# Performance work log

Measured on AMD Instinct MI355X. Metric: run time of the kernel, lower is better.

## Reference

```python
import jax, jax.numpy as jnp
import numpy as np

E, H, B, S = 1024, 16, 8, 512
D = E // H
GRU_BIAS = 2.0  # config['gru_bias']
LN_EPS = 1e-5


def _pos_encoding(seq_len, dim):
    # Transformer-XL style relative positions seq_len-1 .. 0
    pos = jnp.arange(seq_len - 1, -1, -1, dtype=jnp.float32)
    inv_freq = 1.0 / (10000.0 ** (jnp.arange(0, dim, 2, dtype=jnp.float32) / dim))
    ang = pos[:, None] * inv_freq[None, :]              # [S, E/2]
    return jnp.concatenate([jnp.sin(ang), jnp.cos(ang)], axis=-1)  # [S, E]


def _layer_norm(x, g, b):
    m = x.mean(-1, keepdims=True)
    v = ((x - m) ** 2).mean(-1, keepdims=True)
    return (x - m) * jax.lax.rsqrt(v + LN_EPS) * g + b


def _rel_shift(x):
    # x: [B, H, S, S] -> Transformer-XL relative shift
    b, h, s, _ = x.shape
    x = jnp.pad(x, ((0, 0), (0, 0), (0, 0), (1, 0)))
    x = x.reshape(b, h, s + 1, s)[:, :, 1:, :]
    return x


def _gru_gate(x, y, Wr, Ur, Wz, Uz, Wg, Ug):
    # GTrXL gating: r, z gates + candidate h; z biased toward identity by GRU_BIAS
    r = jax.nn.sigmoid(y @ Wr.T + x @ Ur.T)
    z = jax.nn.sigmoid(y @ Wz.T + x @ Uz.T - GRU_BIAS)
    h = jnp.tanh(y @ Wg.T + (r * x) @ Ug.T)
    return (1.0 - z) * x + z * h


def setup_inputs() -> dict:
    rng = jax.random.key(0)
    ks = iter(jax.random.split(rng, 64))
    W = lambda *shape: jax.random.normal(next(ks), shape, jnp.float32) * 0.02
    inp = {
        "query": jax.random.normal(next(ks), (B, S, E), jnp.float32),
        "key": jax.random.normal(next(ks), (B, S, E), jnp.float32),
        "value": jax.random.normal(next(ks), (B, S, E), jnp.float32),
        "mask": jnp.tril(jnp.ones((S, S), dtype=bool)),
        "ln1_g": jnp.ones((E,), jnp.float32), "ln1_b": jnp.zeros((E,), jnp.float32),
        "ln2_g": jnp.ones((E,), jnp.float32), "ln2_b": jnp.zeros((E,), jnp.float32),
        "Wq": W(E, E), "bq": jnp.zeros((E,), jnp.float32),
        "Wk": W(E, E), "bk": jnp.zeros((E,), jnp.float32),
        "Wv": W(E, E), "bv": jnp.zeros((E,), jnp.float32),
        "Wp": W(E, E),
        "Wo": W(E, E), "bo": jnp.zeros((E,), jnp.float32),
        "u_bias": W(H, D), "v_bias": W(H, D),
        "g1_Wr": W(E, E), "g1_Ur": W(E, E), "g1_Wz": W(E, E),
        "g1_Uz": W(E, E), "g1_Wg": W(E, E), "g1_Ug": W(E, E),
        "g2_Wr": W(E, E), "g2_Ur": W(E, E), "g2_Wz": W(E, E),
        "g2_Uz": W(E, E), "g2_Wg": W(E, E), "g2_Ug": W(E, E),
        "fc_W": W(E, E), "fc_b": jnp.zeros((E,), jnp.float32),
    }
    return inp


def reference(query, key, value, mask,
              ln1_g, ln1_b, ln2_g, ln2_b,
              Wq, bq, Wk, bk, Wv, bv, Wp, Wo, bo, u_bias, v_bias,
              g1_Wr, g1_Ur, g1_Wz, g1_Uz, g1_Wg, g1_Ug,
              g2_Wr, g2_Ur, g2_Wz, g2_Uz, g2_Wg, g2_Ug,
              fc_W, fc_b):
    b, s, e = query.shape
    norm_q = _layer_norm(query, ln1_g, ln1_b)
    norm_k = _layer_norm(key, ln1_g, ln1_b)

    q = (norm_q @ Wq.T + bq).reshape(b, s, H, D)
    k = (norm_k @ Wk.T + bk).reshape(b, s, H, D)
    v = (norm_k @ Wv.T + bv).reshape(b, s, H, D)
    r = (_pos_encoding(s, e) @ Wp.T).reshape(s, H, D)      # relative pos keys

    # content term (q + u) k^T and position term (q + v) R^T with rel-shift
    AC = jnp.einsum('bshd,bthd->bhst', q + u_bias, k)
    BD = _rel_shift(jnp.einsum('bshd,thd->bhst', q + v_bias, r))
    score = (AC + BD) / jnp.sqrt(jnp.float32(D))
    score = jnp.where(mask[None, None, :, :], score, jnp.float32(-1e9))
    attn = jax.nn.softmax(score, axis=-1)
    Y = jnp.einsum('bhst,bthd->bshd', attn, v).reshape(b, s, e) @ Wo.T + bo

    out = _gru_gate(query, Y, g1_Wr, g1_Ur, g1_Wz, g1_Uz, g1_Wg, g1_Ug)
    Ef = jax.nn.relu(_layer_norm(out, ln2_g, ln2_b) @ fc_W.T + fc_b)
    out = _gru_gate(out, Ef, g2_Wr, g2_Ur, g2_Wz, g2_Uz, g2_Wg, g2_Ug)
    return out
```

## Files before the change

### kernel.cpp

```cpp
#include <hip/hip_runtime.h>

typedef unsigned short u16;
typedef __attribute__((ext_vector_type(8))) short short8;
typedef __attribute__((ext_vector_type(4))) float f32x4;

#define DEVFN __device__ __forceinline__

constexpr int Bc = 8, Sc = 512, Ec = 1024, Hc = 16, Dc = 64;

DEVFN u16 f2b(float f) {
  union { float f; unsigned u; } a; a.f = f;
  unsigned u = a.u;
  u += 0x7fffu + ((u >> 16) & 1u);
  return (u16)(u >> 16);
}
DEVFN float b2f(u16 h) {
  union { unsigned u; float f; } a; a.u = ((unsigned)h) << 16; return a.f;
}
DEVFN unsigned pack2(float a, float b) {
  return (unsigned)f2b(a) | ((unsigned)f2b(b) << 16);
}
DEVFN float wred_sum(float v) {
  #pragma unroll
  for (int o = 32; o; o >>= 1) v += __shfl_xor(v, o, 64);
  return v;
}
DEVFN void gload16(const void* g, void* l) {
  __builtin_amdgcn_global_load_lds(
      (const __attribute__((address_space(1))) void*)g,
      (__attribute__((address_space(3))) void*)l, 16, 0, 0);
}

struct PtrBundle { const float* src[18]; u16* dst[18]; };

__global__ __launch_bounds__(256) void cvtw_kernel(PtrBundle pb)
{
  int w = blockIdx.y;
  int i = blockIdx.x * 256 + threadIdx.x;
  float4 v = ((const float4*)pb.src[w])[i];
  uint2 o; o.x = pack2(v.x, v.y); o.y = pack2(v.z, v.w);
  ((uint2*)pb.dst[w])[i] = o;
}

struct GemmSeg {
  const u16* A1; const u16* A2;
  const u16* W1; const u16* W2;
  const float* bias;
  const float* bu; const float* bv;
  const u16* xB;
  const float* xF;
  const u16* zB;
  u16* o16a; u16* o16b;
  float* oF;
  int epi;
};
struct GemmDesc { GemmSeg seg[3]; };

template<int TN>
__global__ __launch_bounds__(256) void gemm_f(GemmDesc dd)
{
  constexpr int NI = TN / 32;
  constexpr int BPS = 1024 / TN;
  __shared__ u16 lA[2][128 * 32];
  __shared__ u16 lB[2][TN * 32];
  const int tid = threadIdx.x;

  const GemmSeg s = dd.seg[blockIdx.y / BPS];
  const int n0 = (blockIdx.y % BPS) * TN;
  const int m0 = blockIdx.x * 128;
  const int wid = tid >> 6, lane = tid & 63;
  const int wm = (wid >> 1) * 64, wn = (wid & 1) * (TN / 2);
  const int c15 = lane & 15, g = lane >> 4;
  const int arow = tid >> 2;
  const int ac8 = (((tid & 3) ^ ((tid >> 3) & 3))) * 8;
  const int gs8 = (g ^ ((c15 >> 1) & 3)) * 8;

  f32x4 acc[4][NI];
  #pragma unroll
  for (int mi = 0; mi < 4; ++mi)
    #pragma unroll
    for (int ni = 0; ni < NI; ++ni) acc[mi][ni] = {0.f, 0.f, 0.f, 0.f};

  const int nst = (s.A2 ? 2 : 1) * 32;

  auto stage = [&](int buf, int st) {
    int sg = st >> 5, k0 = (st & 31) << 5;
    const u16* Abase = (sg ? s.A2 : s.A1) + (size_t)m0 * 1024;
    const u16* Wbase = (sg ? s.W2 : s.W1) + (size_t)n0 * 1024;
    gload16(Abase + (size_t)arow * 1024 + k0 + ac8,        &lA[buf][tid * 8]);
    gload16(Abase + (size_t)(arow + 64) * 1024 + k0 + ac8, &lA[buf][2048 + tid * 8]);
    gload16(Wbase + (size_t)arow * 1024 + k0 + ac8,        &lB[buf][tid * 8]);
    if constexpr (TN == 128)
      gload16(Wbase + (size_t)(arow + 64) * 1024 + k0 + ac8, &lB[buf][2048 + tid * 8]);
  };

  stage(0, 0);
  stage(1, 1);

  for (int st = 0; st < nst; ++st) {
    const int cur = st & 1;
    if (st + 1 < nst) {
      if constexpr (TN == 128) asm volatile("s_waitcnt vmcnt(4)" ::: "memory");
      else                     asm volatile("s_waitcnt vmcnt(3)" ::: "memory");
    } else {
      asm volatile("s_waitcnt vmcnt(0)" ::: "memory");
    }
    __builtin_amdgcn_s_barrier();

    short8 afr[4], bfr[NI];
    #pragma unroll
    for (int mi = 0; mi < 4; ++mi)
      afr[mi] = *(const short8*)&lA[cur][(wm + mi * 16 + c15) * 32 + gs8];
    #pragma unroll
    for (int ni = 0; ni < NI; ++ni)
      bfr[ni] = *(const short8*)&lB[cur][(wn + ni * 16 + c15) * 32 + gs8];
    asm volatile("s_waitcnt lgkmcnt(0)" ::: "memory");
    __builtin_amdgcn_sched_barrier(0);
    __builtin_amdgcn_s_barrier();
    __builtin_amdgcn_sched_barrier(0);
    if (st + 2 < nst) stage(cur, st + 2);

    #pragma unroll
    for (int mi = 0; mi < 4; ++mi)
      #pragma unroll
      for (int ni = 0; ni < NI; ++ni)
        acc[mi][ni] = __builtin_amdgcn_mfma_f32_16x16x32_bf16(
            afr[mi], bfr[ni], acc[mi][ni], 0, 0, 0);
  }

  const int colb = n0 + wn + c15;
  const int rowb = m0 + wm + (lane >> 4) * 4;
  #pragma unroll
  for (int ni = 0; ni < NI; ++ni) {
    int col = colb + ni * 16;
    float bb = s.bias ? s.bias[col] : 0.f;
    float bu = 0.f, bvv = 0.f;
    if (s.epi == 1) { bu = s.bu[col]; bvv = s.bv[col]; }
    int hI = col >> 6, dI = col & 63;
    int kcd = (dI >> 5) & 1, gd = (dI >> 3) & 3, ed = dI & 7;
    int ntd = dI >> 4, c15d = dI & 15;
    #pragma unroll
    for (int mi = 0; mi < 4; ++mi) {
      int row0 = rowb + mi * 16;
      size_t off0 = (size_t)row0 * 1024 + col;
      float v4[4];
      #pragma unroll
      for (int q = 0; q < 4; ++q) v4[q] = acc[mi][ni][q] + bb;
      switch (s.epi) {
        case 0:
          #pragma unroll
          for (int q = 0; q < 4; ++q) s.o16a[off0 + (size_t)q * 1024] = f2b(v4[q]);
          break;
        case 1:
          #pragma unroll
          for (int q = 0; q < 4; ++q) {
            int ri = row0 + q;
            size_t off = ((size_t)hI << 18) +
                         (((size_t)(((ri >> 4) * 2 + kcd) * 16 + (ri & 15)) * 4 + gd) << 3) + ed;
            s.o16a[off] = f2b((v4[q] + bu)  * 0.125f);
            s.o16b[off] = f2b((v4[q] + bvv) * 0.125f);
          }
          break;
        case 2:
          #pragma unroll
          for (int q = 0; q < 4; ++q) s.o16a[off0 + (size_t)q * 1024] = f2b(v4[q]);
          break;
        case 3:
          #pragma unroll
          for (int q = 0; q < 4; ++q) {
            size_t off = off0 + (size_t)q * 1024;
            float sg1 = 1.f / (1.f + __expf(-v4[q]));
            s.o16a[off] = f2b(sg1 * b2f(s.xB[off]));
          }
          break;
        case 4:
          #pragma unroll
          for (int q = 0; q < 4; ++q) {
            size_t off = off0 + (size_t)q * 1024;
            float z = 1.f / (1.f + __expf(-(b2f(s.zB[off]) - 2.f)));
            float r = (1.f - z) * s.xF[off] + z * tanhf(v4[q]);
            s.oF[off] = r;
            if (s.o16a) s.o16a[off] = f2b(r);
          }
          break;
        case 5:
          #pragma unroll
          for (int q = 0; q < 4; ++q) s.o16a[off0 + (size_t)q * 1024] = f2b(fmaxf(v4[q], 0.f));
          break;
        case 6: {
          int bI = row0 >> 9, j = row0 & 511;
          int kt = j >> 6, jj = j & 63;
          int kcj = jj >> 5, gj = (jj >> 3) & 3, e0 = jj & 7;
          size_t off = ((size_t)((bI * 16 + hI) * 8 + kt) << 12) +
                       (((size_t)((ntd * 2 + kcj) * 16 + c15d) * 4 + gj) << 3) + e0;
          uint2 o; o.x = pack2(v4[0], v4[1]); o.y = pack2(v4[2], v4[3]);
          *(uint2*)(s.o16a + off) = o;
        } break;
        case 7:
          #pragma unroll
          for (int q = 0; q < 4; ++q) {
            int rj = row0 + q;
            int bI = rj >> 9, kt = (rj >> 6) & 7, jr = rj & 63;
            size_t off = ((size_t)((bI * 16 + hI) * 8 + kt) << 12) +
                         (((size_t)(((jr >> 4) * 2 + kcd) * 16 + (jr & 15)) * 4 + gd) << 3) + ed;
            s.o16a[off] = f2b(v4[q]);
          }
          break;
        case 8:
          #pragma unroll
          for (int q = 0; q < 4; ++q) {
            int t = row0 + q;
            size_t off = ((size_t)hI << 14) +
                         (((size_t)(((t >> 4) * 2 + kcd) * 16 + (t & 15)) * 4 + gd) << 3) + ed;
            s.o16a[off] = f2b(v4[q]);
          }
          break;
      }
    }
  }
}

__global__ __launch_bounds__(256) void ln_kernel(
    const float* __restrict__ x, const float* __restrict__ g,
    const float* __restrict__ bb, u16* __restrict__ out,
    u16* __restrict__ out2)
{
  const int row = blockIdx.x, t = threadIdx.x;
  float4 xv = ((const float4*)x)[(size_t)row * 256 + t];
  float s  = xv.x + xv.y + xv.z + xv.w;
  float s2 = xv.x * xv.x + xv.y * xv.y + xv.z * xv.z + xv.w * xv.w;
  s = wred_sum(s); s2 = wred_sum(s2);
  __shared__ float sh[8];
  int wid = t >> 6, lane = t & 63;
  if (lane == 0) { sh[wid] = s; sh[4 + wid] = s2; }
  __syncthreads();
  s  = sh[0] + sh[1] + sh[2] + sh[3];
  s2 = sh[4] + sh[5] + sh[6] + sh[7];
  float mean = s * (1.f / 1024.f);
  float var  = s2 * (1.f / 1024.f) - mean * mean;
  float rstd = rsqrtf(var + 1e-5f);
  float4 gv = ((const float4*)g)[t];
  float4 bv = ((const float4*)bb)[t];
  uint2 o;
  o.x = pack2((xv.x - mean) * rstd * gv.x + bv.x,
              (xv.y - mean) * rstd * gv.y + bv.y);
  o.y = pack2((xv.z - mean) * rstd * gv.z + bv.z,
              (xv.w - mean) * rstd * gv.w + bv.w);
  *(uint2*)&out[(size_t)row * 1024 + t * 4] = o;
  if (out2) {
    uint2 o2; o2.x = pack2(xv.x, xv.y); o2.y = pack2(xv.z, xv.w);
    *(uint2*)&out2[(size_t)row * 1024 + t * 4] = o2;
  }
}

__global__ __launch_bounds__(256) void posenc_kernel(u16* __restrict__ out)
{
  int idx = blockIdx.x * 256 + threadIdx.x;
  int i = idx >> 9, f = idx & 511;
  float pos = (float)(Sc - 1 - i);
  float invf = expf((float)f * -0.017988946039016f);
  float ang = pos * invf;
  out[(size_t)i * 1024 + f]       = f2b(sinf(ang));
  out[(size_t)i * 1024 + 512 + f] = f2b(cosf(ang));
}

__global__ __launch_bounds__(256) void attn_mfma(
    const u16* __restrict__ quF, const u16* __restrict__ qvF,
    const u16* __restrict__ PK, const u16* __restrict__ PVT,
    const u16* __restrict__ RF, u16* __restrict__ out)
{
  __shared__ u16 lK[2][4096];
  __shared__ u16 lVT[2][4096];
  __shared__ u16 PW[4][16 * 72];

  const int tid = threadIdx.x;
  const int wave = tid >> 6, lane = tid & 63;
  const int g = lane >> 4, c15 = lane & 15;
  const int x = blockIdx.x;
  const int h = blockIdx.y, b = blockIdx.z;
  const int qA = x, qB = 7 - x;

  const size_t pkbase = (size_t)(b * 16 + h) << 15;
  const size_t qhead  = (size_t)h << 18;
  const size_t rhead  = (size_t)h << 14;
  const size_t bh_off = ((size_t)b * Sc) * Ec + h * Dc;
  const int fchunk  = (c15 * 4 + g) * 8;
  const int fchunkS = (c15 * 4 + (g ^ ((c15 >> 1) & 3))) * 8;
  const int src8 = (tid ^ ((tid >> 3) & 3)) * 8;

  u16* pw = PW[wave];

  auto stage = [&](int buf, int kt) {
    const u16* ks = PK  + pkbase + ((size_t)kt << 12);
    const u16* vs = PVT + pkbase + ((size_t)kt << 12);
    gload16(ks + src8,        &lK[buf][tid * 8]);
    gload16(ks + 2048 + src8, &lK[buf][2048 + tid * 8]);
    gload16(vs + src8,        &lVT[buf][tid * 8]);
    gload16(vs + 2048 + src8, &lVT[buf][2048 + tid * 8]);
  };

  short8 qa[2], va[2];
  int i0w = qA * 64 + wave * 16;
  {
    int i16g = b * 32 + (i0w >> 4);
    #pragma unroll
    for (int kc = 0; kc < 2; ++kc) {
      size_t off = qhead + ((size_t)(i16g * 2 + kc) * 64) * 8 + fchunk;
      qa[kc] = *(const short8*)(quF + off);
      va[kc] = *(const short8*)(qvF + off);
    }
  }

  f32x4 oacc[4];
  #pragma unroll
  for (int t = 0; t < 4; ++t) oacc[t] = {0.f, 0.f, 0.f, 0.f};
  float m[4], l[4];
  #pragma unroll
  for (int q = 0; q < 4; ++q) { m[q] = -1e30f; l[q] = 0.f; }

  stage(0, 0);
  asm volatile("s_waitcnt vmcnt(0)" ::: "memory");
  __syncthreads();

  for (int s2 = 0; s2 < 9; ++s2) {
    const int buf = s2 & 1;
    const int kt = (s2 <= x) ? s2 : (s2 - x - 1);
    const int j0 = kt * 64;
    if (s2 < 8) {
      int ns = s2 + 1;
      stage(buf ^ 1, (ns <= x) ? ns : (ns - x - 1));
    }

    f32x4 ac[4];
    #pragma unroll
    for (int t = 0; t < 4; ++t) ac[t] = {0.f, 0.f, 0.f, 0.f};
    __builtin_amdgcn_s_setprio(1);
    #pragma unroll
    for (int kc = 0; kc < 2; ++kc)
      #pragma unroll
      for (int nt = 0; nt < 4; ++nt) {
        short8 kb = *(const short8*)&lK[buf][(nt * 2 + kc) * 512 + fchunkS];
        ac[nt] = __builtin_amdgcn_mfma_f32_16x16x32_bf16(qa[kc], kb, ac[nt], 0, 0, 0);
      }

    const int t016 = (496 - i0w + j0) >> 4;
    f32x4 e5[5];
    #pragma unroll
    for (int t = 0; t < 5; ++t) e5[t] = {0.f, 0.f, 0.f, 0.f};
    #pragma unroll
    for (int kc = 0; kc < 2; ++kc)
      #pragma unroll
      for (int nt = 0; nt < 5; ++nt) {
        int t16 = t016 + nt; t16 = t16 > 31 ? 31 : t16;
        short8 rb = *(const short8*)(RF + rhead + (size_t)(t16 * 2 + kc) * 512 + fchunk);
        e5[nt] = __builtin_amdgcn_mfma_f32_16x16x32_bf16(va[kc], rb, e5[nt], 0, 0, 0);
      }
    __builtin_amdgcn_s_setprio(0);

    float rot[5][4];
    #pragma unroll
    for (int q = 0; q < 4; ++q) {
      int src = (lane & 48) | ((15 - (g * 4 + q) + c15) & 15);
      #pragma unroll
      for (int nt = 0; nt < 5; ++nt)
        rot[nt][q] = __shfl(e5[nt][q], src, 64);
    }

    float s[4][4];
    #pragma unroll
    for (int ct = 0; ct < 4; ++ct) {
      int jcol = j0 + ct * 16 + c15;
      #pragma unroll
      for (int q = 0; q < 4; ++q) {
        int r = g * 4 + q;
        int u = 15 - r + c15;
        float bd = (u >> 4) ? rot[ct + 1][q] : rot[ct][q];
        float sv = ac[ct][q] + bd;
        s[ct][q] = (jcol <= i0w + r) ? sv : -1e30f;
      }
    }

    float mnew[4], csc[4];
    #pragma unroll
    for (int q = 0; q < 4; ++q) {
      float mx = fmaxf(fmaxf(s[0][q], s[1][q]), fmaxf(s[2][q], s[3][q]));
      #pragma unroll
      for (int o = 8; o; o >>= 1) mx = fmaxf(mx, __shfl_xor(mx, o, 64));
      mnew[q] = fmaxf(m[q], mx);
      csc[q] = __expf(m[q] - mnew[q]);
      m[q] = mnew[q];
    }
    float rs[4] = {0.f, 0.f, 0.f, 0.f};
    float p[4][4];
    #pragma unroll
    for (int ct = 0; ct < 4; ++ct)
      #pragma unroll
      for (int q = 0; q < 4; ++q) {
        p[ct][q] = __expf(s[ct][q] - mnew[q]);
        rs[q] += p[ct][q];
      }
    #pragma unroll
    for (int q = 0; q < 4; ++q) {
      float t = rs[q];
      #pragma unroll
      for (int o = 8; o; o >>= 1) t += __shfl_xor(t, o, 64);
      l[q] = l[q] * csc[q] + t;
      #pragma unroll
      for (int ct = 0; ct < 4; ++ct) oacc[ct][q] *= csc[q];
    }

    #pragma unroll
    for (int ct = 0; ct < 4; ++ct)
      #pragma unroll
      for (int q = 0; q < 4; ++q)
        pw[(g * 4 + q) * 72 + ct * 16 + c15] = f2b(p[ct][q]);

    __builtin_amdgcn_s_setprio(1);
    #pragma unroll
    for (int kc = 0; kc < 2; ++kc) {
      short8 pa = *(const short8*)&pw[c15 * 72 + kc * 32 + g * 8];
      #pragma unroll
      for (int nt = 0; nt < 4; ++nt) {
        short8 vb8 = *(const short8*)&lVT[buf][(nt * 2 + kc) * 512 + fchunkS];
        oacc[nt] = __builtin_amdgcn_mfma_f32_16x16x32_bf16(pa, vb8, oacc[nt], 0, 0, 0);
      }
    }
    __builtin_amdgcn_s_setprio(0);

    if (s2 == x) {
      #pragma unroll
      for (int q = 0; q < 4; ++q) {
        float rl = 1.f / l[q];
        size_t ro = bh_off + (size_t)(i0w + g * 4 + q) * Ec;
        #pragma unroll
        for (int ct = 0; ct < 4; ++ct)
          out[ro + ct * 16 + c15] = f2b(oacc[ct][q] * rl);
      }
      i0w = qB * 64 + wave * 16;
      int i16g = b * 32 + (i0w >> 4);
      #pragma unroll
      for (int kc = 0; kc < 2; ++kc) {
        size_t off = qhead + ((size_t)(i16g * 2 + kc) * 64) * 8 + fchunk;
        qa[kc] = *(const short8*)(quF + off);
        va[kc] = *(const short8*)(qvF + off);
      }
      #pragma unroll
      for (int t = 0; t < 4; ++t) oacc[t] = {0.f, 0.f, 0.f, 0.f};
      #pragma unroll
      for (int q = 0; q < 4; ++q) { m[q] = -1e30f; l[q] = 0.f; }
    }

    asm volatile("s_waitcnt vmcnt(0)" ::: "memory");
    __syncthreads();
  }

  #pragma unroll
  for (int q = 0; q < 4; ++q) {
    float rl = 1.f / l[q];
    size_t ro = bh_off + (size_t)(i0w + g * 4 + q) * Ec;
    #pragma unroll
    for (int ct = 0; ct < 4; ++ct)
      out[ro + ct * 16 + c15] = f2b(oacc[ct][q] * rl);
  }
}

extern "C" void kernel_launch(void* const* d_in, const int* in_sizes, int n_in,
                              void* d_out, int out_size, void* d_ws, size_t ws_size,
                              hipStream_t stream) {
  (void)in_sizes; (void)n_in; (void)out_size; (void)ws_size;

  const float* query = (const float*)d_in[0];
  const float* key   = (const float*)d_in[1];
  const float* ln1_g = (const float*)d_in[4];
  const float* ln1_b = (const float*)d_in[5];
  const float* ln2_g = (const float*)d_in[6];
  const float* ln2_b = (const float*)d_in[7];
  const float* Wq = (const float*)d_in[8];   const float* bq = (const float*)d_in[9];
  const float* Wk = (const float*)d_in[10];  const float* bk = (const float*)d_in[11];
  const float* Wv = (const float*)d_in[12];  const float* bv_in = (const float*)d_in[13];
  const float* Wp = (const float*)d_in[14];
  const float* Wo = (const float*)d_in[15];  const float* bo = (const float*)d_in[16];
  const float* u_bias = (const float*)d_in[17];
  const float* v_bias = (const float*)d_in[18];
  const float* fc_W = (const float*)d_in[31]; const float* fc_b = (const float*)d_in[32];

  const size_t MB = 1ull << 20;
  char* ws = (char*)d_ws;
  u16* wb[18];
  for (int i = 0; i < 18; ++i) wb[i] = (u16*)(ws + (size_t)i * 2 * MB);
  u16*   normq16 = (u16*)(ws + 36 * MB);
  u16*   normk16 = (u16*)(ws + 44 * MB);
  u16*   xq16    = (u16*)(ws + 52 * MB);
  u16*   pos16   = (u16*)(ws + 60 * MB);
  u16*   rF16    = (u16*)(ws + 61 * MB);
  u16*   quF16   = (u16*)(ws + 62 * MB);
  u16*   qvF16   = (u16*)(ws + 70 * MB);
  u16*   pk16    = (u16*)(ws + 78 * MB);
  u16*   pvt16   = (u16*)(ws + 86 * MB);
  float* out1    = (float*)(ws + 94 * MB);
  u16*   att16   = normq16;
  u16*   Y16     = normk16;
  u16*   rx16    = normq16;
  u16*   out116  = quF16;
  u16*   Ef16    = qvF16;
  u16*   ln2o16  = xq16;
  u16*   tB16    = pk16;

  PtrBundle pb;
  const float* wsrc[18] = {Wq, Wk, Wv, Wp, Wo, fc_W,
                           (const float*)d_in[19], (const float*)d_in[20],
                           (const float*)d_in[21], (const float*)d_in[22],
                           (const float*)d_in[23], (const float*)d_in[24],
                           (const float*)d_in[25], (const float*)d_in[26],
                           (const float*)d_in[27], (const float*)d_in[28],
                           (const float*)d_in[29], (const float*)d_in[30]};
  for (int i = 0; i < 18; ++i) { pb.src[i] = wsrc[i]; pb.dst[i] = wb[i]; }
  cvtw_kernel<<<dim3(1024, 18), 256, 0, stream>>>(pb);

  ln_kernel<<<4096, 256, 0, stream>>>(query, ln1_g, ln1_b, normq16, xq16);
  ln_kernel<<<4096, 256, 0, stream>>>(key,   ln1_g, ln1_b, normk16, nullptr);
  posenc_kernel<<<1024, 256, 0, stream>>>(pos16);

  GemmSeg z{}; GemmDesc d;

  d.seg[0] = z; d.seg[0].A1 = normq16; d.seg[0].W1 = wb[0]; d.seg[0].bias = bq;
  d.seg[0].bu = u_bias; d.seg[0].bv = v_bias;
  d.seg[0].o16a = quF16; d.seg[0].o16b = qvF16; d.seg[0].epi = 1;
  d.seg[1] = z; d.seg[1].A1 = normk16; d.seg[1].W1 = wb[1]; d.seg[1].bias = bk;
  d.seg[1].o16a = pk16; d.seg[1].epi = 7;
  d.seg[2] = z; d.seg[2].A1 = normk16; d.seg[2].W1 = wb[2]; d.seg[2].bias = bv_in;
  d.seg[2].o16a = pvt16; d.seg[2].epi = 6;
  gemm_f<128><<<dim3(32, 24), 256, 0, stream>>>(d);

  d.seg[0] = z; d.seg[0].A1 = pos16; d.seg[0].W1 = wb[3];
  d.seg[0].o16a = rF16; d.seg[0].epi = 8;
  gemm_f<64><<<dim3(4, 16), 256, 0, stream>>>(d);

  attn_mfma<<<dim3(4, 16, 8), 256, 0, stream>>>(quF16, qvF16, pk16, pvt16,
                                                rF16, att16);

  d.seg[0] = z; d.seg[0].A1 = att16; d.seg[0].W1 = wb[4]; d.seg[0].bias = bo;
  d.seg[0].o16a = Y16; d.seg[0].epi = 0;
  gemm_f<64><<<dim3(32, 16), 256, 0, stream>>>(d);

  d.seg[0] = z; d.seg[0].A1 = Y16; d.seg[0].A2 = xq16;
  d.seg[0].W1 = wb[6]; d.seg[0].W2 = wb[7];
  d.seg[0].xB = xq16; d.seg[0].o16a = rx16; d.seg[0].epi = 3;
  d.seg[1] = z; d.seg[1].A1 = Y16; d.seg[1].A2 = xq16;
  d.seg[1].W1 = wb[8]; d.seg[1].W2 = wb[9];
  d.seg[1].o16a = tB16; d.seg[1].epi = 2;
  gemm_f<128><<<dim3(32, 16), 256, 0, stream>>>(d);

  d.seg[0] = z; d.seg[0].A1 = Y16; d.seg[0].A2 = rx16;
  d.seg[0].W1 = wb[10]; d.seg[0].W2 = wb[11];
  d.seg[0].xF = query; d.seg[0].zB = tB16;
  d.seg[0].oF = out1; d.seg[0].o16a = out116; d.seg[0].epi = 4;
  gemm_f<64><<<dim3(32, 16), 256, 0, stream>>>(d);

  ln_kernel<<<4096, 256, 0, stream>>>(out1, ln2_g, ln2_b, ln2o16, nullptr);
  d.seg[0] = z; d.seg[0].A1 = ln2o16; d.seg[0].W1 = wb[5]; d.seg[0].bias = fc_b;
  d.seg[0].o16a = Ef16; d.seg[0].epi = 5;
  gemm_f<64><<<dim3(32, 16), 256, 0, stream>>>(d);

  d.seg[0] = z; d.seg[0].A1 = Ef16; d.seg[0].A2 = out116;
  d.seg[0].W1 = wb[12]; d.seg[0].W2 = wb[13];
  d.seg[0].xB = out116; d.seg[0].o16a = rx16; d.seg[0].epi = 3;
  d.seg[1] = z; d.seg[1].A1 = Ef16; d.seg[1].A2 = out116;
  d.seg[1].W1 = wb[14]; d.seg[1].W2 = wb[15];
  d.seg[1].o16a = tB16; d.seg[1].epi = 2;
  gemm_f<128><<<dim3(32, 16), 256, 0, stream>>>(d);

  d.seg[0] = z; d.seg[0].A1 = Ef16; d.seg[0].A2 = rx16;
  d.seg[0].W1 = wb[16]; d.seg[0].W2 = wb[17];
  d.seg[0].xF = out1; d.seg[0].zB = tB16;
  d.seg[0].oF = (float*)d_out; d.seg[0].epi = 4;
  gemm_f<64><<<dim3(32, 16), 256, 0, stream>>>(d);
}
```

Before: 386.6 us.

## Restructure GEMM: deeper multi-buffer pipeline, smaller warp tiles, more blocks

Result: faster. 329.2 us (-14.8%).

```diff
diff --git a/kernel.cpp b/kernel.cpp
--- a/kernel.cpp
+++ b/kernel.cpp
@@ -56,30 +56,34 @@
 };
 struct GemmDesc { GemmSeg seg[3]; };
 
-template<int TN>
-__global__ __launch_bounds__(256) void gemm_f(GemmDesc dd)
+template<int TM, int TN>
+__global__ __launch_bounds__(TM == 128 ? 512 : 256) void gemm_f(GemmDesc dd)
 {
-  constexpr int NI = TN / 32;
+  constexpr int MI = TM / 32;
+  constexpr int D = (TM == 128) ? 2 : 3;
+  constexpr int NBUF = D + 1;
   constexpr int BPS = 1024 / TN;
-  __shared__ u16 lA[2][128 * 32];
-  __shared__ u16 lB[2][TN * 32];
+  __shared__ u16 lA[NBUF][TM * 32];
+  __shared__ u16 lB[NBUF][TN * 32];
   const int tid = threadIdx.x;
 
   const GemmSeg s = dd.seg[blockIdx.y / BPS];
   const int n0 = (blockIdx.y % BPS) * TN;
-  const int m0 = blockIdx.x * 128;
+  const int m0 = blockIdx.x * TM;
   const int wid = tid >> 6, lane = tid & 63;
-  const int wm = (wid >> 1) * 64, wn = (wid & 1) * (TN / 2);
+  int wm, wn;
+  if constexpr (TM == 128) { wm = (wid >> 2) * 64; wn = (wid & 3) * 32; }
+  else                     { wm = (wid >> 1) * 32; wn = (wid & 1) * 32; }
   const int c15 = lane & 15, g = lane >> 4;
   const int arow = tid >> 2;
   const int ac8 = (((tid & 3) ^ ((tid >> 3) & 3))) * 8;
   const int gs8 = (g ^ ((c15 >> 1) & 3)) * 8;
 
-  f32x4 acc[4][NI];
-  #pragma unroll
-  for (int mi = 0; mi < 4; ++mi)
-    #pragma unroll
-    for (int ni = 0; ni < NI; ++ni) acc[mi][ni] = {0.f, 0.f, 0.f, 0.f};
+  f32x4 acc[MI][2];
+  #pragma unroll
+  for (int mi = 0; mi < MI; ++mi)
+    #pragma unroll
+    for (int ni = 0; ni < 2; ++ni) acc[mi][ni] = {0.f, 0.f, 0.f, 0.f};
 
   const int nst = (s.A2 ? 2 : 1) * 32;
 
@@ -87,43 +91,40 @@
     int sg = st >> 5, k0 = (st & 31) << 5;
     const u16* Abase = (sg ? s.A2 : s.A1) + (size_t)m0 * 1024;
     const u16* Wbase = (sg ? s.W2 : s.W1) + (size_t)n0 * 1024;
-    gload16(Abase + (size_t)arow * 1024 + k0 + ac8,        &lA[buf][tid * 8]);
-    gload16(Abase + (size_t)(arow + 64) * 1024 + k0 + ac8, &lA[buf][2048 + tid * 8]);
-    gload16(Wbase + (size_t)arow * 1024 + k0 + ac8,        &lB[buf][tid * 8]);
-    if constexpr (TN == 128)
-      gload16(Wbase + (size_t)(arow + 64) * 1024 + k0 + ac8, &lB[buf][2048 + tid * 8]);
+    gload16(Abase + (size_t)arow * 1024 + k0 + ac8, &lA[buf][tid * 8]);
+    gload16(Wbase + (size_t)arow * 1024 + k0 + ac8, &lB[buf][tid * 8]);
   };
 
-  stage(0, 0);
-  stage(1, 1);
+  #pragma unroll
+  for (int p = 0; p < D; ++p) stage(p, p);
 
   for (int st = 0; st < nst; ++st) {
-    const int cur = st & 1;
-    if (st + 1 < nst) {
-      if constexpr (TN == 128) asm volatile("s_waitcnt vmcnt(4)" ::: "memory");
-      else                     asm volatile("s_waitcnt vmcnt(3)" ::: "memory");
+    const int cur = st % NBUF;
+    if constexpr (D == 2) {
+      if (st + 1 < nst) asm volatile("s_waitcnt vmcnt(2)" ::: "memory");
+      else              asm volatile("s_waitcnt vmcnt(0)" ::: "memory");
     } else {
-      asm volatile("s_waitcnt vmcnt(0)" ::: "memory");
-    }
-    __builtin_amdgcn_s_barrier();
-
-    short8 afr[4], bfr[NI];
-    #pragma unroll
-    for (int mi = 0; mi < 4; ++mi)
-      afr[mi] = *(const short8*)&lA[cur][(wm + mi * 16 + c15) * 32 + gs8];
-    #pragma unroll
-    for (int ni = 0; ni < NI; ++ni)
-      bfr[ni] = *(const short8*)&lB[cur][(wn + ni * 16 + c15) * 32 + gs8];
-    asm volatile("s_waitcnt lgkmcnt(0)" ::: "memory");
-    __builtin_amdgcn_sched_barrier(0);
+      if (st + 2 < nst)      asm volatile("s_waitcnt vmcnt(4)" ::: "memory");
+      else if (st + 1 < nst) asm volatile("s_waitcnt vmcnt(2)" ::: "memory");
+      else                   asm volatile("s_waitcnt vmcnt(0)" ::: "memory");
+    }
     __builtin_amdgcn_s_barrier();
     __builtin_amdgcn_sched_barrier(0);
-    if (st + 2 < nst) stage(cur, st + 2);
-
-    #pragma unroll
-    for (int mi = 0; mi < 4; ++mi)
-      #pragma unroll
-      for (int ni = 0; ni < NI; ++ni)
+
+    short8 afr[MI], bfr[2];
+    #pragma unroll
+    for (int mi = 0; mi < MI; ++mi)
+      afr[mi] = *(const short8*)&lA[cur][(wm + mi * 16 + c15) * 32 + gs8];
+    #pragma unroll
+    for (int ni = 0; ni < 2; ++ni)
+      bfr[ni] = *(const short8*)&lB[cur][(wn + ni * 16 + c15) * 32 + gs8];
+
+    if (st + D < nst) stage((st + D) % NBUF, st + D);
+
+    #pragma unroll
+    for (int mi = 0; mi < MI; ++mi)
+      #pragma unroll
+      for (int ni = 0; ni < 2; ++ni)
         acc[mi][ni] = __builtin_amdgcn_mfma_f32_16x16x32_bf16(
             afr[mi], bfr[ni], acc[mi][ni], 0, 0, 0);
   }
@@ -131,7 +132,7 @@
   const int colb = n0 + wn + c15;
   const int rowb = m0 + wm + (lane >> 4) * 4;
   #pragma unroll
-  for (int ni = 0; ni < NI; ++ni) {
+  for (int ni = 0; ni < 2; ++ni) {
     int col = colb + ni * 16;
     float bb = s.bias ? s.bias[col] : 0.f;
     float bu = 0.f, bvv = 0.f;
@@ -140,7 +141,7 @@
     int kcd = (dI >> 5) & 1, gd = (dI >> 3) & 3, ed = dI & 7;
     int ntd = dI >> 4, c15d = dI & 15;
     #pragma unroll
-    for (int mi = 0; mi < 4; ++mi) {
+    for (int mi = 0; mi < MI; ++mi) {
       int row0 = rowb + mi * 16;
       size_t off0 = (size_t)row0 * 1024 + col;
       float v4[4];
@@ -530,18 +531,18 @@
   d.seg[1].o16a = pk16; d.seg[1].epi = 7;
   d.seg[2] = z; d.seg[2].A1 = normk16; d.seg[2].W1 = wb[2]; d.seg[2].bias = bv_in;
   d.seg[2].o16a = pvt16; d.seg[2].epi = 6;
-  gemm_f<128><<<dim3(32, 24), 256, 0, stream>>>(d);
+  gemm_f<128, 128><<<dim3(32, 24), 512, 0, stream>>>(d);
 
   d.seg[0] = z; d.seg[0].A1 = pos16; d.seg[0].W1 = wb[3];
   d.seg[0].o16a = rF16; d.seg[0].epi = 8;
-  gemm_f<64><<<dim3(4, 16), 256, 0, stream>>>(d);
+  gemm_f<64, 64><<<dim3(8, 16), 256, 0, stream>>>(d);
 
   attn_mfma<<<dim3(4, 16, 8), 256, 0, stream>>>(quF16, qvF16, pk16, pvt16,
                                                 rF16, att16);
 
   d.seg[0] = z; d.seg[0].A1 = att16; d.seg[0].W1 = wb[4]; d.seg[0].bias = bo;
   d.seg[0].o16a = Y16; d.seg[0].epi = 0;
-  gemm_f<64><<<dim3(32, 16), 256, 0, stream>>>(d);
+  gemm_f<64, 64><<<dim3(64, 16), 256, 0, stream>>>(d);
 
   d.seg[0] = z; d.seg[0].A1 = Y16; d.seg[0].A2 = xq16;
   d.seg[0].W1 = wb[6]; d.seg[0].W2 = wb[7];
@@ -549,18 +550,18 @@
   d.seg[1] = z; d.seg[1].A1 = Y16; d.seg[1].A2 = xq16;
   d.seg[1].W1 = wb[8]; d.seg[1].W2 = wb[9];
   d.seg[1].o16a = tB16; d.seg[1].epi = 2;
-  gemm_f<128><<<dim3(32, 16), 256, 0, stream>>>(d);
+  gemm_f<128, 128><<<dim3(32, 16), 512, 0, stream>>>(d);
 
   d.seg[0] = z; d.seg[0].A1 = Y16; d.seg[0].A2 = rx16;
   d.seg[0].W1 = wb[10]; d.seg[0].W2 = wb[11];
   d.seg[0].xF = query; d.seg[0].zB = tB16;
   d.seg[0].oF = out1; d.seg[0].o16a = out116; d.seg[0].epi = 4;
-  gemm_f<64><<<dim3(32, 16), 256, 0, stream>>>(d);
+  gemm_f<64, 64><<<dim3(64, 16), 256, 0, stream>>>(d);
 
   ln_kernel<<<4096, 256, 0, stream>>>(out1, ln2_g, ln2_b, ln2o16, nullptr);
   d.seg[0] = z; d.seg[0].A1 = ln2o16; d.seg[0].W1 = wb[5]; d.seg[0].bias = fc_b;
   d.seg[0].o16a = Ef16; d.seg[0].epi = 5;
-  gemm_f<64><<<dim3(32, 16), 256, 0, stream>>>(d);
+  gemm_f<64, 64><<<dim3(64, 16), 256, 0, stream>>>(d);
 
   d.seg[0] = z; d.seg[0].A1 = Ef16; d.seg[0].A2 = out116;
   d.seg[0].W1 = wb[12]; d.seg[0].W2 = wb[13];
@@ -568,11 +569,11 @@
   d.seg[1] = z; d.seg[1].A1 = Ef16; d.seg[1].A2 = out116;
   d.seg[1].W1 = wb[14]; d.seg[1].W2 = wb[15];
   d.seg[1].o16a = tB16; d.seg[1].epi = 2;
-  gemm_f<128><<<dim3(32, 16), 256, 0, stream>>>(d);
+  gemm_f<128, 128><<<dim3(32, 16), 512, 0, stream>>>(d);
 
   d.seg[0] = z; d.seg[0].A1 = Ef16; d.seg[0].A2 = rx16;
   d.seg[0].W1 = wb[16]; d.seg[0].W2 = wb[17];
   d.seg[0].xF = out1; d.seg[0].zB = tB16;
   d.seg[0].oF = (float*)d_out; d.seg[0].epi = 4;
-  gemm_f<64><<<dim3(32, 16), 256, 0, stream>>>(d);
-}
+  gemm_f<64, 64><<<dim3(64, 16), 256, 0, stream>>>(d);
+}
```
